# Performance work log

Measured on AMD Instinct MI355X. Metric: run time of the kernel, lower is better.

The kernel has to match this reference:

```python
import jax, jax.numpy as jnp
import numpy as np

N, E, D = 50000, 300000, 64
ETYPES = ['temporal', 'assigned_to', 'com', 'tin', 'win', 'sin', 'take_time', 'use_time']


def setup_inputs():
    key = jax.random.key(0)
    ks = iter(jax.random.split(key, 80))

    def nrm(shape, s=1.0):
        return jax.random.normal(next(ks), shape, dtype=jnp.float32) * s

    inp = {}
    inp['feat_task'] = nrm((N, D))
    inp['feat_worker'] = nrm((N, D))
    inp['feat_state'] = nrm((N, D))
    for et in ETYPES:
        inp['src_' + et] = jax.random.randint(next(ks), (E,), 0, N, dtype=jnp.int32)
        inp['dst_' + et] = jax.random.randint(next(ks), (E,), 0, N, dtype=jnp.int32)
    inp['w_temporal'] = jax.random.uniform(next(ks), (E, 1), dtype=jnp.float32)
    inp['t_take_time'] = jax.random.uniform(next(ks), (E, 1), dtype=jnp.float32)
    inp['t_use_time'] = jax.random.uniform(next(ks), (E, 1), dtype=jnp.float32)
    for et in ETYPES:
        inp['W_' + et] = nrm((D, D), 0.05)
        inp['b_' + et] = nrm((D,), 0.05)
    for nm in ['edge_fc', 'edge_fc_ttr', 'edge_fc_rut']:
        inp[nm + '_W'] = nrm((D, 1), 0.05)
        inp[nm + '_b'] = nrm((D,), 0.05)
    inp['attn_W'] = nrm((1, 3 * D), 0.05)
    inp['attn_ttr_W'] = nrm((1, 3 * D), 0.05)
    inp['attn_rut_W'] = nrm((1, 3 * D), 0.05)
    inp['attn_assigned_W'] = nrm((1, 2 * D), 0.05)
    inp['attn_com_W'] = nrm((1, 2 * D), 0.05)
    inp['attn_tin_W'] = nrm((1, 2 * D), 0.05)
    inp['attn_rin_W'] = nrm((1, 2 * D), 0.05)
    return inp


def _seg_softmax_sum(e, msg, dst, n):
    # numerically stable segment softmax over each dst node's incoming edges,
    # followed by the alpha-weighted scatter-sum (DGL reduce_func).
    m = jax.ops.segment_max(e, dst, num_segments=n)        # [n,1]
    ex = jnp.exp(e - m[dst])                               # [E,1]
    den = jax.ops.segment_sum(ex, dst, num_segments=n)     # [n,1]
    return jax.ops.segment_sum((ex / den[dst]) * msg, dst, num_segments=n)


def _gat(Wh_s, Wh_d, src, dst, aW, n, zij=None):
    # e = leaky_relu(attn_fc(concat(z_src, z_dst[, zij]))); the concat is never
    # materialized -- attn weight is split into per-block dot products.
    d = Wh_s.shape[1]
    zs = Wh_s[src]
    e = zs @ aW[0, :d] + Wh_d[dst] @ aW[0, d:2 * d]
    if zij is not None:
        e = e + zij @ aW[0, 2 * d:]
        msg = zs + zij   # message_func: src Wh + edge embedding
    else:
        msg = zs
    e = jax.nn.leaky_relu(e, 0.2)[:, None]
    return _seg_softmax_sum(e, msg, dst, n)


def _forward(feat_task, feat_worker, feat_state, w_temporal, t_take_time, t_use_time,
             W_temporal, b_temporal, W_assigned_to, b_assigned_to, W_com, b_com,
             W_tin, b_tin, W_win, b_win, W_sin, b_sin, W_take_time, b_take_time,
             W_use_time, b_use_time, edge_fc_W, edge_fc_b, edge_fc_ttr_W, edge_fc_ttr_b,
             edge_fc_rut_W, edge_fc_rut_b, attn_W, attn_assigned_W, attn_com_W,
             attn_tin_W, attn_rin_W, attn_ttr_W, attn_rut_W,
             src_temporal, dst_temporal, src_assigned_to, dst_assigned_to,
             src_com, dst_com, src_tin, dst_tin, src_win, dst_win,
             src_sin, dst_sin, src_take_time, dst_take_time, src_use_time, dst_use_time):
    n_task, n_worker, n_state = feat_task.shape[0], feat_worker.shape[0], feat_state.shape[0]
    # Equation (1): per-etype linear projection of source node features
    Wh_temporal = feat_task @ W_temporal.T + b_temporal
    Wh_assigned = feat_task @ W_assigned_to.T + b_assigned_to
    Wh_com = feat_worker @ W_com.T + b_com
    Wh_tin = feat_task @ W_tin.T + b_tin
    Wh_win = feat_worker @ W_win.T + b_win
    Wh_sin = feat_state @ W_sin.T + b_sin
    Wh_ttr = feat_task @ W_take_time.T + b_take_time
    Wh_rut = feat_worker @ W_use_time.T + b_use_time
    # per-edge scalar feature -> d-dim embedding
    zij_t = w_temporal @ edge_fc_W.T + edge_fc_b
    zij_ttr = t_take_time @ edge_fc_ttr_W.T + edge_fc_ttr_b
    zij_rut = t_use_time @ edge_fc_rut_W.T + edge_fc_rut_b
    # Equations (2)-(4): per-etype attention + segment softmax + scatter-sum
    h_temporal = _gat(Wh_temporal, Wh_temporal, src_temporal, dst_temporal, attn_W, n_task, zij_t)
    h_assigned = _gat(Wh_assigned, Wh_com, src_assigned_to, dst_assigned_to, attn_assigned_W, n_worker)
    h_com = _gat(Wh_com, Wh_com, src_com, dst_com, attn_com_W, n_worker)
    h_tin = _gat(Wh_tin, Wh_sin, src_tin, dst_tin, attn_tin_W, n_state)
    h_win = _gat(Wh_win, Wh_sin, src_win, dst_win, attn_rin_W, n_state)
    h_sin = jax.ops.segment_sum(Wh_sin[src_sin], dst_sin, num_segments=n_state)  # copy_src + sum
    h_ttr = _gat(Wh_ttr, Wh_com, src_take_time, dst_take_time, attn_ttr_W, n_worker, zij_ttr)
    h_rut = _gat(Wh_rut, Wh_temporal, src_use_time, dst_use_time, attn_rut_W, n_task, zij_rut)
    # multi_update_all cross-type 'sum', then ReLU
    h_task = jax.nn.relu(h_temporal + h_rut)
    h_worker = jax.nn.relu(h_assigned + h_com + h_ttr)
    h_state = jax.nn.relu(h_tin + h_win + h_sin)
    return jnp.stack([h_task, h_worker, h_state])  # [3, N, D]


def reference(feat_task, feat_worker, feat_state,
              src_temporal, dst_temporal, src_assigned_to, dst_assigned_to,
              src_com, dst_com, src_tin, dst_tin, src_win, dst_win,
              src_sin, dst_sin, src_take_time, dst_take_time, src_use_time, dst_use_time,
              w_temporal, t_take_time, t_use_time,
              W_temporal, b_temporal, W_assigned_to, b_assigned_to, W_com, b_com,
              W_tin, b_tin, W_win, b_win, W_sin, b_sin, W_take_time, b_take_time,
              W_use_time, b_use_time, edge_fc_W, edge_fc_b, edge_fc_ttr_W, edge_fc_ttr_b,
              edge_fc_rut_W, edge_fc_rut_b, attn_W, attn_ttr_W, attn_rut_W,
              attn_assigned_W, attn_com_W, attn_tin_W, attn_rin_W):
    return _forward(feat_task, feat_worker, feat_state, w_temporal, t_take_time, t_use_time,
                    W_temporal, b_temporal, W_assigned_to, b_assigned_to, W_com, b_com,
                    W_tin, b_tin, W_win, b_win, W_sin, b_sin, W_take_time, b_take_time,
                    W_use_time, b_use_time, edge_fc_W, edge_fc_b, edge_fc_ttr_W, edge_fc_ttr_b,
                    edge_fc_rut_W, edge_fc_rut_b, attn_W, attn_assigned_W, attn_com_W,
                    attn_tin_W, attn_rin_W, attn_ttr_W, attn_rut_W,
                    src_temporal, dst_temporal, src_assigned_to, dst_assigned_to,
                    src_com, dst_com, src_tin, dst_tin, src_win, dst_win,
                    src_sin, dst_sin, src_take_time, dst_take_time, src_use_time, dst_use_time)
```

## Files before the change

### kernel.cpp

```cpp
#include <hip/hip_runtime.h>
#include <math.h>

#define NN 50000
#define EE 300000
#define NG 8
#define NTOT (NG * NN)
#define NBKT 782
#define BCAP 3584
#define TILE 1024
#define NBLKE ((EE + TILE - 1) / TILE)

typedef unsigned short u16;
typedef unsigned int u32;
typedef short bf16x8 __attribute__((ext_vector_type(8)));
typedef float f32x16 __attribute__((ext_vector_type(16)));

__device__ __forceinline__ float b2f(u16 u) { return __uint_as_float(((u32)u) << 16); }
__device__ __forceinline__ u16 f2b(float f) {
    u32 x = __float_as_uint(f);
    u32 lsb = (x >> 16) & 1u;
    return (u16)((x + 0x7fffu + lsb) >> 16);
}

__global__ void HeteroGATLayer_14259291423309_kernel() {}

struct SetupP {
    int* gcur;
    const float* attn[3]; const float* fcW[3]; const float* fcb[3];
    float* consts;
};

__global__ __launch_bounds__(256) void k_setup(SetupP p) {
    const int i = blockIdx.x * 256 + threadIdx.x;
    if (i < NBKT) p.gcur[i] = 0;
    if (blockIdx.x == 3) {
        const int z = threadIdx.x >> 6, lane = threadIdx.x & 63;
        if (z < 3) {
            float a2 = p.attn[z][128 + lane];
            float x = p.fcW[z][lane] * a2;
            float y = p.fcb[z][lane] * a2;
            #pragma unroll
            for (int off = 32; off; off >>= 1) {
                x += __shfl_down(x, off);
                y += __shfl_down(y, off);
            }
            if (lane == 0) {
                const int co[3] = {0, 10, 12};
                p.consts[co[z]] = x;
                p.consts[co[z] + 1] = y;
            }
        }
    }
}

struct ProjP {
    const float* feat[3];
    const float* W[8]; const float* b[8];
    u16* wh;
    int ntile[3]; int tiles[3][4];
    int nvec[8];
    const float* avec[8][4];
    float* dvec[8][4];
};

__global__ __launch_bounds__(256) void k_proj(ProjP p) {
    __shared__ u16 sA[64 * 64];
    __shared__ u16 sW[64 * 64];
    __shared__ u16 sC[64 * 66];
    const int f = blockIdx.y;
    const int tid = threadIdx.x;
    const int row0 = blockIdx.x * 64;
    const float* feat = p.feat[f];

    #pragma unroll
    for (int q = 0; q < 4; ++q) {
        int idx = q * 256 + tid;
        int r = idx >> 4;
        int c4 = (idx & 15) * 4;
        int gr = row0 + r;
        if (gr >= NN) gr = NN - 1;
        float4 fv = *(const float4*)(feat + (size_t)gr * 64 + c4);
        *(ushort4*)&sA[r * 64 + c4] = make_ushort4(f2b(fv.x), f2b(fv.y), f2b(fv.z), f2b(fv.w));
    }

    const int wv = tid >> 6, lane = tid & 63;
    const int mrow = (wv & 1) * 32, ncol = (wv >> 1) * 32;
    const int half = lane >> 5, l31 = lane & 31;
    const int nt = p.ntile[f];

    for (int ti = 0; ti < nt; ++ti) {
        const int t = p.tiles[f][ti];
        const float* W = p.W[t];
        #pragma unroll
        for (int q = 0; q < 4; ++q) {
            int idx = q * 256 + tid;
            int r = idx >> 4;
            int c4 = (idx & 15) * 4;
            float4 wv4 = *(const float4*)(W + r * 64 + c4);
            *(ushort4*)&sW[r * 64 + c4] = make_ushort4(f2b(wv4.x), f2b(wv4.y), f2b(wv4.z), f2b(wv4.w));
        }
        __syncthreads();

        f32x16 acc;
        #pragma unroll
        for (int i = 0; i < 16; ++i) acc[i] = 0.0f;
        #pragma unroll
        for (int k0 = 0; k0 < 64; k0 += 16) {
            bf16x8 af = *(const bf16x8*)&sA[(mrow + l31) * 64 + k0 + half * 8];
            bf16x8 bf = *(const bf16x8*)&sW[(ncol + l31) * 64 + k0 + half * 8];
            acc = __builtin_amdgcn_mfma_f32_32x32x16_bf16(af, bf, acc, 0, 0, 0);
        }

        float bb = p.b[t][ncol + l31];
        u16* whp = p.wh + (size_t)t * NN * 64;
        #pragma unroll
        for (int reg = 0; reg < 16; ++reg) {
            int rowD = (reg & 3) + 8 * (reg >> 2) + 4 * half;
            int gr = row0 + mrow + rowD;
            u16 c16 = f2b(acc[reg] + bb);
            if (gr < NN) whp[(size_t)gr * 64 + ncol + l31] = c16;
            sC[(mrow + rowD) * 66 + ncol + l31] = c16;
        }
        __syncthreads();

        const int r = tid & 63, j = tid >> 6;
        if (j < p.nvec[t]) {
            const float* av = p.avec[t][j];
            float s = 0.f;
            #pragma unroll
            for (int c = 0; c < 64; c += 4) {
                ushort4 cv = *(const ushort4*)&sC[r * 66 + c];
                float4 a4 = *(const float4*)(av + c);
                s += b2f(cv.x) * a4.x + b2f(cv.y) * a4.y + b2f(cv.z) * a4.z + b2f(cv.w) * a4.w;
            }
            int gr = row0 + r;
            if (gr < NN) p.dvec[t][j][gr] = s;
        }
    }
}

struct BinAP {
    const int* src[8]; const int* dst[8]; const float* w[8];
    const float* el[8]; const float* er[8];
    const float* consts;
    int whoff[8];
    int* gcur; int4* bkt;
};

__global__ __launch_bounds__(256) void k_binA(BinAP p) {
    __shared__ int hist[128];
    const int g = blockIdx.y;
    const int b0 = (g * NN) >> 9;
    const int tid = threadIdx.x;
    const int e = blockIdx.x * TILE + tid * 4;
    if (tid < 128) hist[tid] = 0;

    const bool hw = p.w[g] != 0;
    float c1 = 0.f, c0 = 0.f;
    if (g < 7 && hw) { c1 = p.consts[2 * g]; c0 = p.consts[2 * g + 1]; }
    const int wo = p.whoff[g];

    int sr[4], bl[4], low[4];
    float sc[4], pw[4];
    const bool valid = e < EE;
    if (valid) {
        int4 s4 = *(const int4*)(p.src[g] + e);
        int4 d4 = *(const int4*)(p.dst[g] + e);
        float4 w4 = make_float4(0.f, 0.f, 0.f, 0.f);
        if (hw) w4 = *(const float4*)(p.w[g] + e);
        int ss[4] = {s4.x, s4.y, s4.z, s4.w};
        int dd[4] = {d4.x, d4.y, d4.z, d4.w};
        float ww[4] = {w4.x, w4.y, w4.z, w4.w};
        #pragma unroll
        for (int q = 0; q < 4; ++q) {
            int key = g * NN + dd[q];
            bl[q] = (key >> 9) - b0;
            low[q] = key & 511;
            sr[q] = wo + (ss[q] << 7);
            float scv = 1.0f, pwv = 0.0f;
            if (g < 7) {
                scv = p.el[g][ss[q]] + p.er[g][dd[q]];
                if (hw) scv += c1 * ww[q] + c0;
                scv = scv > 0.f ? scv : 0.2f * scv;
                scv = __expf(scv);
                if (hw) pwv = scv * ww[q];
            }
            sc[q] = scv; pw[q] = pwv;
        }
    }
    __syncthreads();
    if (valid) {
        #pragma unroll
        for (int q = 0; q < 4; ++q) atomicAdd(&hist[bl[q]], 1);
    }
    __syncthreads();
    if (tid < 128) {
        int c = hist[tid];
        hist[tid] = c ? atomicAdd(&p.gcur[b0 + tid], c) : 0;
    }
    __syncthreads();
    if (valid) {
        #pragma unroll
        for (int q = 0; q < 4; ++q) {
            int pos = atomicAdd(&hist[bl[q]], 1);
            int4 v;
            v.x = sr[q];
            v.y = __float_as_int(sc[q]);
            v.z = __float_as_int(pw[q]);
            v.w = low[q];
            p.bkt[(size_t)(b0 + bl[q]) * BCAP + pos] = v;
        }
    }
}

__global__ __launch_bounds__(512) void k_binB(const int* __restrict__ gcur,
                                              const int4* __restrict__ bkt,
                                              int2* __restrict__ csr,
                                              int4* __restrict__ rowdeg) {
    __shared__ int2 st2[BCAP];
    __shared__ float st3[BCAP];
    __shared__ int hist[512];
    __shared__ int scn[512];
    __shared__ int wsum[8];
    const int b = blockIdx.x;
    const int tid = threadIdx.x;
    int count = gcur[b];
    if (count > BCAP) count = BCAP;
    hist[tid] = 0;
    __syncthreads();
    const int4* src = bkt + (size_t)b * BCAP;
    for (int i = tid; i < count; i += 512) atomicAdd(&hist[src[i].w], 1);
    __syncthreads();
    int h = hist[tid];
    const int lane = tid & 63, wvi = tid >> 6;
    int incl = h;
    #pragma unroll
    for (int off = 1; off < 64; off <<= 1) {
        int t = __shfl_up(incl, off);
        if (lane >= off) incl += t;
    }
    if (lane == 63) wsum[wvi] = incl;
    __syncthreads();
    int wb = 0;
    #pragma unroll
    for (int w = 0; w < 8; ++w)
        if (w < wvi) wb += wsum[w];
    const int excl = wb + incl - h;
    scn[tid] = excl;
    __syncthreads();
    for (int i = tid; i < count; i += 512) {
        int4 v = src[i];
        int pos = atomicAdd(&scn[v.w], 1);
        st2[pos] = make_int2(v.x, v.y);
        st3[pos] = __int_as_float(v.z);
    }
    __syncthreads();
    float den = 0.f, sw = 0.f;
    for (int j = 0; j < h; ++j) {
        den += __int_as_float(st2[excl + j].y);
        sw += st3[excl + j];
    }
    const int gkey = b * 512 + tid;
    if (gkey < NTOT) {
        float inv = (gkey >= 7 * NN) ? 1.0f : ((h > 0 && den > 0.f) ? 1.0f / den : 0.f);
        u32 beg = (u32)(b * BCAP + excl);
        rowdeg[gkey] = make_int4((int)((beg << 10) | (u32)h),
                                 __float_as_int(inv), __float_as_int(sw * inv), 0);
    }
    for (int i = tid; i < count; i += 512) csr[(size_t)b * BCAP + i] = st2[i];
}

struct GathP {
    int gidx[3][3]; int hasfc[3][3];
    const float* fcW[3][3]; const float* fcb[3][3];
};

__device__ __forceinline__ void chunk_acc(const char* whA, int dby, int2 v, int len,
                                          float& vs0, float& vs1) {
    int myS = v.x;
    float mySc = __int_as_float(v.y);
    int k = 0;
    for (; k + 4 <= len; k += 4) {
        int s0 = __shfl(myS, k), s1 = __shfl(myS, k + 1);
        int s2 = __shfl(myS, k + 2), s3 = __shfl(myS, k + 3);
        float a0 = __shfl(mySc, k), a1 = __shfl(mySc, k + 1);
        float a2 = __shfl(mySc, k + 2), a3 = __shfl(mySc, k + 3);
        vs0 += a0 * b2f(*(const u16*)(whA + (u32)(s0 + dby)));
        vs1 += a1 * b2f(*(const u16*)(whA + (u32)(s1 + dby)));
        vs0 += a2 * b2f(*(const u16*)(whA + (u32)(s2 + dby)));
        vs1 += a3 * b2f(*(const u16*)(whA + (u32)(s3 + dby)));
    }
    for (; k < len; ++k) {
        int s = __shfl(myS, k);
        float a = __shfl(mySc, k);
        vs0 += a * b2f(*(const u16*)(whA + (u32)(s + dby)));
    }
}

#define GSTEP4(t, segP)                                                            \
    {                                                                              \
        int2 e0 = segP[k], e1 = segP[k + 1], e2 = segP[k + 2], e3 = segP[k + 3];   \
        const u16* q0 = (const u16*)(whA + (u32)(e0.x + dby));                     \
        const u16* q1 = (const u16*)(whA + (u32)(e1.x + dby));                     \
        const u16* q2 = (const u16*)(whA + (u32)(e2.x + dby));                     \
        const u16* q3 = (const u16*)(whA + (u32)(e3.x + dby));                     \
        float x0 = b2f(*q0), x1 = b2f(*q1), x2 = b2f(*q2), x3 = b2f(*q3);          \
        vs0[t] += __int_as_float(e0.y) * x0;                                       \
        vs1[t] += __int_as_float(e1.y) * x1;                                       \
        vs0[t] += __int_as_float(e2.y) * x2;                                       \
        vs1[t] += __int_as_float(e3.y) * x3;                                       \
    }

__global__ __launch_bounds__(256) void k_gather(GathP p,
        const int4* __restrict__ rowdeg, const int2* __restrict__ csr,
        const char* __restrict__ whA, float* __restrict__ out) {
    __shared__ int2 sSeg[4][3][64];
    const int tg = blockIdx.y;
    const int wv = threadIdx.x >> 6, d = threadIdx.x & 63;
    const int i = blockIdx.x * 4 + wv;
    const int dby = 2 * d;
    const int ng = (tg == 0) ? 2 : 3;

    int len[3]; u32 beg[3]; float inv[3], sw[3];
    #pragma unroll
    for (int t = 0; t < 3; ++t) {
        len[t] = 0; beg[t] = 0; inv[t] = 0.f; sw[t] = 0.f;
        if (t < ng) {
            int4 rv = rowdeg[p.gidx[tg][t] * NN + i];
            int rx = __builtin_amdgcn_readfirstlane(rv.x);
            len[t] = rx & 1023;
            beg[t] = ((u32)rx) >> 10;
            inv[t] = __uint_as_float((u32)__builtin_amdgcn_readfirstlane(rv.y));
            sw[t] = __uint_as_float((u32)__builtin_amdgcn_readfirstlane(rv.z));
        }
    }
    #pragma unroll
    for (int t = 0; t < 3; ++t) {
        int2 v = (d < len[t]) ? csr[beg[t] + d] : make_int2(0, 0);
        sSeg[wv][t][d] = v;
    }
    const int2* sp0 = sSeg[wv][0];
    const int2* sp1 = sSeg[wv][1];
    const int2* sp2 = sSeg[wv][2];

    const int l0 = len[0] < 64 ? len[0] : 64;
    const int l1 = len[1] < 64 ? len[1] : 64;
    const int l2 = len[2] < 64 ? len[2] : 64;
    int kmax = l0 > l1 ? l0 : l1;
    kmax = kmax > l2 ? kmax : l2;

    float vs0[3] = {0.f, 0.f, 0.f}, vs1[3] = {0.f, 0.f, 0.f};
    for (int k = 0; k < kmax; k += 4) {
        if (k < l0) GSTEP4(0, sp0)
        if (k < l1) GSTEP4(1, sp1)
        if (k < l2) GSTEP4(2, sp2)
    }
    #pragma unroll
    for (int t = 0; t < 3; ++t) {
        if (len[t] > 64) {
            for (u32 base = beg[t] + 64; base < beg[t] + (u32)len[t]; base += 64) {
                int len2 = (int)(beg[t] + (u32)len[t] - base);
                if (len2 > 64) len2 = 64;
                int2 v = (d < len2) ? csr[base + d] : make_int2(0, 0);
                chunk_acc(whA, dby, v, len2, vs0[t], vs1[t]);
            }
        }
    }

    float tot = 0.f;
    #pragma unroll
    for (int t = 0; t < 3; ++t) {
        if (len[t] == 0) continue;
        tot += (vs0[t] + vs1[t]) * inv[t];
        if (p.hasfc[tg][t])
            tot += p.fcW[tg][t][d] * sw[t] + p.fcb[tg][t][d];
    }
    out[((size_t)tg * NN + i) * 64 + d] = tot > 0.f ? tot : 0.f;
}

extern "C" void kernel_launch(void* const* d_in, const int* in_sizes, int n_in,
                              void* d_out, int out_size, void* d_ws, size_t ws_size,
                              hipStream_t stream) {
    (void)in_sizes; (void)n_in; (void)out_size; (void)ws_size;
    const float* feats[3] = {(const float*)d_in[0], (const float*)d_in[1], (const float*)d_in[2]};
    const int* srcs[8];
    const int* dsts[8];
    for (int t = 0; t < 8; ++t) {
        srcs[t] = (const int*)d_in[3 + 2 * t];
        dsts[t] = (const int*)d_in[4 + 2 * t];
    }
    const float* ew0 = (const float*)d_in[19];
    const float* ew1 = (const float*)d_in[20];
    const float* ew2 = (const float*)d_in[21];
    const float* Wm[8];
    const float* bm[8];
    for (int t = 0; t < 8; ++t) {
        Wm[t] = (const float*)d_in[22 + 2 * t];
        bm[t] = (const float*)d_in[23 + 2 * t];
    }
    const float* fcW0 = (const float*)d_in[38];
    const float* fcb0 = (const float*)d_in[39];
    const float* fcW1 = (const float*)d_in[40];
    const float* fcb1 = (const float*)d_in[41];
    const float* fcW2 = (const float*)d_in[42];
    const float* fcb2 = (const float*)d_in[43];
    const float* attn_W          = (const float*)d_in[44];
    const float* attn_ttr_W      = (const float*)d_in[45];
    const float* attn_rut_W      = (const float*)d_in[46];
    const float* attn_assigned_W = (const float*)d_in[47];
    const float* attn_com_W      = (const float*)d_in[48];
    const float* attn_tin_W      = (const float*)d_in[49];
    const float* attn_rin_W      = (const float*)d_in[50];

    u16* Wh = (u16*)d_ws;
    char* b0 = (char*)d_ws + (size_t)8 * NN * 64 * sizeof(u16);
    float* el     = (float*)b0;
    float* er     = el + (size_t)7 * NN;
    float* consts = er + (size_t)7 * NN;
    int* gcur     = (int*)(consts + 16);
    int4* rowdeg4 = (int4*)(((size_t)(gcur + NBKT) + 15) & ~(size_t)15);
    int4* bkt     = rowdeg4 + NTOT;
    int2* csr     = (int2*)(bkt + (size_t)NBKT * BCAP);

    int g_et[8]   = {0, 1, 2, 3, 4, 6, 7, 5};
    int g_sidx[8] = {0, 1, 2, 3, 4, 6, 7, 5};
    const float* g_w[8] = {ew0, 0, 0, 0, 0, ew1, ew2, 0};

    {
        SetupP sp;
        sp.gcur = gcur;
        sp.attn[0] = attn_W;     sp.fcW[0] = fcW0; sp.fcb[0] = fcb0;
        sp.attn[1] = attn_ttr_W; sp.fcW[1] = fcW1; sp.fcb[1] = fcb1;
        sp.attn[2] = attn_rut_W; sp.fcW[2] = fcW2; sp.fcb[2] = fcb2;
        sp.consts = consts;
        k_setup<<<4, 256, 0, stream>>>(sp);
    }

    {
        ProjP pp;
        pp.feat[0] = feats[0]; pp.feat[1] = feats[1]; pp.feat[2] = feats[2];
        for (int t = 0; t < 8; ++t) { pp.W[t] = Wm[t]; pp.b[t] = bm[t]; }
        pp.wh = Wh;
        pp.ntile[0] = 4; pp.tiles[0][0] = 0; pp.tiles[0][1] = 1; pp.tiles[0][2] = 3; pp.tiles[0][3] = 6;
        pp.ntile[1] = 3; pp.tiles[1][0] = 2; pp.tiles[1][1] = 4; pp.tiles[1][2] = 7; pp.tiles[1][3] = 0;
        pp.ntile[2] = 1; pp.tiles[2][0] = 5; pp.tiles[2][1] = 0; pp.tiles[2][2] = 0; pp.tiles[2][3] = 0;
        for (int t = 0; t < 8; ++t) {
            pp.nvec[t] = 0;
            for (int j = 0; j < 4; ++j) { pp.avec[t][j] = 0; pp.dvec[t][j] = 0; }
        }
        auto setv = [&](int t, int j, const float* a, float* dv) { pp.avec[t][j] = a; pp.dvec[t][j] = dv; };
        pp.nvec[0] = 3; setv(0, 0, attn_W, el);           setv(0, 1, attn_W + 64, er);
                        setv(0, 2, attn_rut_W + 64, er + 6 * NN);
        pp.nvec[1] = 1; setv(1, 0, attn_assigned_W, el + 1 * NN);
        pp.nvec[2] = 4; setv(2, 0, attn_com_W, el + 2 * NN); setv(2, 1, attn_assigned_W + 64, er + 1 * NN);
                        setv(2, 2, attn_com_W + 64, er + 2 * NN); setv(2, 3, attn_ttr_W + 64, er + 5 * NN);
        pp.nvec[3] = 1; setv(3, 0, attn_tin_W, el + 3 * NN);
        pp.nvec[4] = 1; setv(4, 0, attn_rin_W, el + 4 * NN);
        pp.nvec[5] = 2; setv(5, 0, attn_tin_W + 64, er + 3 * NN); setv(5, 1, attn_rin_W + 64, er + 4 * NN);
        pp.nvec[6] = 1; setv(6, 0, attn_ttr_W, el + 5 * NN);
        pp.nvec[7] = 1; setv(7, 0, attn_rut_W, el + 6 * NN);
        k_proj<<<dim3(782, 3), 256, 0, stream>>>(pp);
    }

    {
        BinAP bp;
        for (int g = 0; g < 8; ++g) {
            bp.src[g] = srcs[g_et[g]];
            bp.dst[g] = dsts[g_et[g]];
            bp.w[g] = g_w[g];
            bp.el[g] = (g < 7) ? el + (size_t)g * NN : 0;
            bp.er[g] = (g < 7) ? er + (size_t)g * NN : 0;
            bp.whoff[g] = g_sidx[g] * NN * 128;
        }
        bp.consts = consts;
        bp.gcur = gcur;
        bp.bkt = bkt;
        k_binA<<<dim3(NBLKE, 8), 256, 0, stream>>>(bp);
    }
    k_binB<<<NBKT, 512, 0, stream>>>(gcur, bkt, csr, rowdeg4);

    {
        GathP gp;
        gp.gidx[0][0] = 0; gp.hasfc[0][0] = 1; gp.fcW[0][0] = fcW0; gp.fcb[0][0] = fcb0;
        gp.gidx[0][1] = 6; gp.hasfc[0][1] = 1; gp.fcW[0][1] = fcW2; gp.fcb[0][1] = fcb2;
        gp.gidx[0][2] = 0; gp.hasfc[0][2] = 0; gp.fcW[0][2] = 0;    gp.fcb[0][2] = 0;
        gp.gidx[1][0] = 1; gp.hasfc[1][0] = 0; gp.fcW[1][0] = 0;    gp.fcb[1][0] = 0;
        gp.gidx[1][1] = 2; gp.hasfc[1][1] = 0; gp.fcW[1][1] = 0;    gp.fcb[1][1] = 0;
        gp.gidx[1][2] = 5; gp.hasfc[1][2] = 1; gp.fcW[1][2] = fcW1; gp.fcb[1][2] = fcb1;
        gp.gidx[2][0] = 3; gp.hasfc[2][0] = 0; gp.fcW[2][0] = 0;    gp.fcb[2][0] = 0;
        gp.gidx[2][1] = 4; gp.hasfc[2][1] = 0; gp.fcW[2][1] = 0;    gp.fcb[2][1] = 0;
        gp.gidx[2][2] = 7; gp.hasfc[2][2] = 0; gp.fcW[2][2] = 0;    gp.fcb[2][2] = 0;
        k_gather<<<dim3(NN / 4, 3), 256, 0, stream>>>(gp, rowdeg4, csr,
                                                      (const char*)Wh, (float*)d_out);
    }
}
```

Measured before the change: 370.8 us.

## Pack two destination rows per wavefront with 32-bit bf16 pair loads

The gather kernel now maps each half-wavefront (32 lanes) to its own destination row, and each lane handles two adjacent feature columns through one 32-bit load of a packed bf16 pair and a float2 store. The separate shuffle-based overflow path for rows longer than 64 is replaced by a unified chunked loop that stages both halves' edge lists in shared memory. This aims to halve the number of load instructions and double the rows per block. The cost is that both halves iterate to the longer of their two edge counts, which adds divergence on uneven degrees.

```diff
diff --git a/kernel.cpp b/kernel.cpp
--- a/kernel.cpp
+++ b/kernel.cpp
@@ -275,107 +275,102 @@
     const float* fcW[3][3]; const float* fcb[3][3];
 };
 
-__device__ __forceinline__ void chunk_acc(const char* whA, int dby, int2 v, int len,
-                                          float& vs0, float& vs1) {
-    int myS = v.x;
-    float mySc = __int_as_float(v.y);
-    int k = 0;
-    for (; k + 4 <= len; k += 4) {
-        int s0 = __shfl(myS, k), s1 = __shfl(myS, k + 1);
-        int s2 = __shfl(myS, k + 2), s3 = __shfl(myS, k + 3);
-        float a0 = __shfl(mySc, k), a1 = __shfl(mySc, k + 1);
-        float a2 = __shfl(mySc, k + 2), a3 = __shfl(mySc, k + 3);
-        vs0 += a0 * b2f(*(const u16*)(whA + (u32)(s0 + dby)));
-        vs1 += a1 * b2f(*(const u16*)(whA + (u32)(s1 + dby)));
-        vs0 += a2 * b2f(*(const u16*)(whA + (u32)(s2 + dby)));
-        vs1 += a3 * b2f(*(const u16*)(whA + (u32)(s3 + dby)));
-    }
-    for (; k < len; ++k) {
-        int s = __shfl(myS, k);
-        float a = __shfl(mySc, k);
-        vs0 += a * b2f(*(const u16*)(whA + (u32)(s + dby)));
-    }
-}
-
-#define GSTEP4(t, segP)                                                            \
+#define GSTEP4(t, sp)                                                              \
     {                                                                              \
-        int2 e0 = segP[k], e1 = segP[k + 1], e2 = segP[k + 2], e3 = segP[k + 3];   \
-        const u16* q0 = (const u16*)(whA + (u32)(e0.x + dby));                     \
-        const u16* q1 = (const u16*)(whA + (u32)(e1.x + dby));                     \
-        const u16* q2 = (const u16*)(whA + (u32)(e2.x + dby));                     \
-        const u16* q3 = (const u16*)(whA + (u32)(e3.x + dby));                     \
-        float x0 = b2f(*q0), x1 = b2f(*q1), x2 = b2f(*q2), x3 = b2f(*q3);          \
-        vs0[t] += __int_as_float(e0.y) * x0;                                       \
-        vs1[t] += __int_as_float(e1.y) * x1;                                       \
-        vs0[t] += __int_as_float(e2.y) * x2;                                       \
-        vs1[t] += __int_as_float(e3.y) * x3;                                       \
+        int2 e0 = sp[k], e1 = sp[k + 1], e2 = sp[k + 2], e3 = sp[k + 3];           \
+        u32 w0 = *(const u32*)(whA + (u32)(e0.x + dby));                           \
+        u32 w1 = *(const u32*)(whA + (u32)(e1.x + dby));                           \
+        u32 w2 = *(const u32*)(whA + (u32)(e2.x + dby));                           \
+        u32 w3 = *(const u32*)(whA + (u32)(e3.x + dby));                           \
+        acc0[t] += __int_as_float(e0.y) * b2f((u16)w0);                            \
+        acc1[t] += __int_as_float(e0.y) * b2f((u16)(w0 >> 16));                    \
+        acc0[t] += __int_as_float(e1.y) * b2f((u16)w1);                            \
+        acc1[t] += __int_as_float(e1.y) * b2f((u16)(w1 >> 16));                    \
+        acc0[t] += __int_as_float(e2.y) * b2f((u16)w2);                            \
+        acc1[t] += __int_as_float(e2.y) * b2f((u16)(w2 >> 16));                    \
+        acc0[t] += __int_as_float(e3.y) * b2f((u16)w3);                            \
+        acc1[t] += __int_as_float(e3.y) * b2f((u16)(w3 >> 16));                    \
     }
 
 __global__ __launch_bounds__(256) void k_gather(GathP p,
         const int4* __restrict__ rowdeg, const int2* __restrict__ csr,
         const char* __restrict__ whA, float* __restrict__ out) {
-    __shared__ int2 sSeg[4][3][64];
+    __shared__ int2 sSeg[4][3][2][64];
     const int tg = blockIdx.y;
-    const int wv = threadIdx.x >> 6, d = threadIdx.x & 63;
-    const int i = blockIdx.x * 4 + wv;
-    const int dby = 2 * d;
+    const int wv = threadIdx.x >> 6, lane = threadIdx.x & 63;
+    const int half = lane >> 5, c = lane & 31;
+    const int i = blockIdx.x * 8 + wv * 2 + half;
+    const int dby = c * 4;
     const int ng = (tg == 0) ? 2 : 3;
 
-    int len[3]; u32 beg[3]; float inv[3], sw[3];
+    int lenv[3]; u32 begv[3]; float invv[3], swv[3];
     #pragma unroll
     for (int t = 0; t < 3; ++t) {
-        len[t] = 0; beg[t] = 0; inv[t] = 0.f; sw[t] = 0.f;
+        lenv[t] = 0; begv[t] = 0; invv[t] = 0.f; swv[t] = 0.f;
         if (t < ng) {
             int4 rv = rowdeg[p.gidx[tg][t] * NN + i];
-            int rx = __builtin_amdgcn_readfirstlane(rv.x);
-            len[t] = rx & 1023;
-            beg[t] = ((u32)rx) >> 10;
-            inv[t] = __uint_as_float((u32)__builtin_amdgcn_readfirstlane(rv.y));
-            sw[t] = __uint_as_float((u32)__builtin_amdgcn_readfirstlane(rv.z));
-        }
-    }
+            lenv[t] = rv.x & 1023;
+            begv[t] = ((u32)rv.x) >> 10;
+            invv[t] = __int_as_float(rv.y);
+            swv[t] = __int_as_float(rv.z);
+        }
+    }
+    int lenA[3], lenB[3], lmax[3]; u32 begA[3], begB[3];
     #pragma unroll
     for (int t = 0; t < 3; ++t) {
-        int2 v = (d < len[t]) ? csr[beg[t] + d] : make_int2(0, 0);
-        sSeg[wv][t][d] = v;
-    }
-    const int2* sp0 = sSeg[wv][0];
-    const int2* sp1 = sSeg[wv][1];
-    const int2* sp2 = sSeg[wv][2];
-
-    const int l0 = len[0] < 64 ? len[0] : 64;
-    const int l1 = len[1] < 64 ? len[1] : 64;
-    const int l2 = len[2] < 64 ? len[2] : 64;
-    int kmax = l0 > l1 ? l0 : l1;
-    kmax = kmax > l2 ? kmax : l2;
-
-    float vs0[3] = {0.f, 0.f, 0.f}, vs1[3] = {0.f, 0.f, 0.f};
-    for (int k = 0; k < kmax; k += 4) {
-        if (k < l0) GSTEP4(0, sp0)
-        if (k < l1) GSTEP4(1, sp1)
-        if (k < l2) GSTEP4(2, sp2)
-    }
+        lenA[t] = __builtin_amdgcn_readlane(lenv[t], 0);
+        lenB[t] = __builtin_amdgcn_readlane(lenv[t], 32);
+        begA[t] = (u32)__builtin_amdgcn_readlane((int)begv[t], 0);
+        begB[t] = (u32)__builtin_amdgcn_readlane((int)begv[t], 32);
+        lmax[t] = lenA[t] > lenB[t] ? lenA[t] : lenB[t];
+    }
+    int kall = lmax[0] > lmax[1] ? lmax[0] : lmax[1];
+    kall = kall > lmax[2] ? kall : lmax[2];
+
+    float acc0[3] = {0.f, 0.f, 0.f}, acc1[3] = {0.f, 0.f, 0.f};
+    for (int cb = 0; cb < kall; cb += 64) {
+        #pragma unroll
+        for (int t = 0; t < 3; ++t) {
+            if (cb < lmax[t]) {
+                int2 vA = (lane < lenA[t] - cb) ? csr[begA[t] + cb + lane] : make_int2(0, 0);
+                sSeg[wv][t][0][lane] = vA;
+                int2 vB = (lane < lenB[t] - cb) ? csr[begB[t] + cb + lane] : make_int2(0, 0);
+                sSeg[wv][t][1][lane] = vB;
+            }
+        }
+        const int2* s0 = sSeg[wv][0][half];
+        const int2* s1 = sSeg[wv][1][half];
+        const int2* s2 = sSeg[wv][2][half];
+        int l0 = lmax[0] - cb, l1 = lmax[1] - cb, l2 = lmax[2] - cb;
+        if (l0 > 64) l0 = 64;
+        if (l1 > 64) l1 = 64;
+        if (l2 > 64) l2 = 64;
+        int cmax = l0 > l1 ? l0 : l1;
+        cmax = cmax > l2 ? cmax : l2;
+        for (int k = 0; k < cmax; k += 4) {
+            if (k < l0) GSTEP4(0, s0)
+            if (k < l1) GSTEP4(1, s1)
+            if (k < l2) GSTEP4(2, s2)
+        }
+    }
+
+    float tot0 = 0.f, tot1 = 0.f;
     #pragma unroll
     for (int t = 0; t < 3; ++t) {
-        if (len[t] > 64) {
-            for (u32 base = beg[t] + 64; base < beg[t] + (u32)len[t]; base += 64) {
-                int len2 = (int)(beg[t] + (u32)len[t] - base);
-                if (len2 > 64) len2 = 64;
-                int2 v = (d < len2) ? csr[base + d] : make_int2(0, 0);
-                chunk_acc(whA, dby, v, len2, vs0[t], vs1[t]);
-            }
-        }
-    }
-
-    float tot = 0.f;
-    #pragma unroll
-    for (int t = 0; t < 3; ++t) {
-        if (len[t] == 0) continue;
-        tot += (vs0[t] + vs1[t]) * inv[t];
-        if (p.hasfc[tg][t])
-            tot += p.fcW[tg][t][d] * sw[t] + p.fcb[tg][t][d];
-    }
-    out[((size_t)tg * NN + i) * 64 + d] = tot > 0.f ? tot : 0.f;
+        tot0 += acc0[t] * invv[t];
+        tot1 += acc1[t] * invv[t];
+        if (p.hasfc[tg][t]) {
+            bool he = lenv[t] > 0;
+            float2 fw = *(const float2*)(p.fcW[tg][t] + 2 * c);
+            float2 fb = *(const float2*)(p.fcb[tg][t] + 2 * c);
+            tot0 += he ? (fw.x * swv[t] + fb.x) : 0.f;
+            tot1 += he ? (fw.y * swv[t] + fb.y) : 0.f;
+        }
+    }
+    float2 o;
+    o.x = tot0 > 0.f ? tot0 : 0.f;
+    o.y = tot1 > 0.f ? tot1 : 0.f;
+    *(float2*)(out + ((size_t)tg * NN + i) * 64 + 2 * c) = o;
 }
 
 extern "C" void kernel_launch(void* const* d_in, const int* in_sizes, int n_in,
@@ -483,14 +478,14 @@
         GathP gp;
         gp.gidx[0][0] = 0; gp.hasfc[0][0] = 1; gp.fcW[0][0] = fcW0; gp.fcb[0][0] = fcb0;
         gp.gidx[0][1] = 6; gp.hasfc[0][1] = 1; gp.fcW[0][1] = fcW2; gp.fcb[0][1] = fcb2;
-        gp.gidx[0][2] = 0; gp.hasfc[0][2] = 0; gp.fcW[0][2] = 0;    gp.fcb[0][2] = 0;
-        gp.gidx[1][0] = 1; gp.hasfc[1][0] = 0; gp.fcW[1][0] = 0;    gp.fcb[1][0] = 0;
-        gp.gidx[1][1] = 2; gp.hasfc[1][1] = 0; gp.fcW[1][1] = 0;    gp.fcb[1][1] = 0;
+        gp.gidx[0][2] = 0; gp.hasfc[0][2] = 0; gp.fcW[0][2] = fcW0; gp.fcb[0][2] = fcb0;
+        gp.gidx[1][0] = 1; gp.hasfc[1][0] = 0; gp.fcW[1][0] = fcW0; gp.fcb[1][0] = fcb0;
+        gp.gidx[1][1] = 2; gp.hasfc[1][1] = 0; gp.fcW[1][1] = fcW0; gp.fcb[1][1] = fcb0;
         gp.gidx[1][2] = 5; gp.hasfc[1][2] = 1; gp.fcW[1][2] = fcW1; gp.fcb[1][2] = fcb1;
-        gp.gidx[2][0] = 3; gp.hasfc[2][0] = 0; gp.fcW[2][0] = 0;    gp.fcb[2][0] = 0;
-        gp.gidx[2][1] = 4; gp.hasfc[2][1] = 0; gp.fcW[2][1] = 0;    gp.fcb[2][1] = 0;
-        gp.gidx[2][2] = 7; gp.hasfc[2][2] = 0; gp.fcW[2][2] = 0;    gp.fcb[2][2] = 0;
-        k_gather<<<dim3(NN / 4, 3), 256, 0, stream>>>(gp, rowdeg4, csr,
+        gp.gidx[2][0] = 3; gp.hasfc[2][0] = 0; gp.fcW[2][0] = fcW0; gp.fcb[2][0] = fcb0;
+        gp.gidx[2][1] = 4; gp.hasfc[2][1] = 0; gp.fcW[2][1] = fcW0; gp.fcb[2][1] = fcb0;
+        gp.gidx[2][2] = 7; gp.hasfc[2][2] = 0; gp.fcW[2][2] = fcW0; gp.fcb[2][2] = fcb0;
+        k_gather<<<dim3(NN / 8, 3), 256, 0, stream>>>(gp, rowdeg4, csr,
                                                       (const char*)Wh, (float*)d_out);
     }
 }
```

Measured after the change: 345.9 us. 1.07x faster.
